# Optimization experiments

Measured on AMD Instinct MI355X. Metric: run time of the kernel, lower is better.

Reference implementation:

```python
import jax, jax.numpy as jnp
import numpy as np

E = 100_000      # number of edges
KMAX = 16        # neighbors (quadruplet basis edges) per edge, exact in this setup
E_NB = E * KMAX  # total neighbor entries
D_EDGE, D_SBF, D_QUAD = 128, 32, 32
INV_SQRT_2 = 0.7071067811865475


def setup_inputs() -> dict:
    key = jax.random.key(0)
    ks = jax.random.split(key, 8)
    m_st = jax.random.normal(ks[0], (E, D_EDGE), dtype=jnp.float32)
    sbf = jax.random.normal(ks[1], (E_NB, D_SBF), dtype=jnp.float32)
    # consistent ragged structure: each edge has exactly KMAX neighbor entries
    edge_nb_idx = jnp.repeat(jnp.arange(E, dtype=jnp.int64), KMAX)
    edge_nb_ragged_idx = jnp.tile(jnp.arange(KMAX, dtype=jnp.int64), E)
    idx_swap = jax.random.permutation(ks[2], E).astype(jnp.int64)
    # parameters (Dense layers are bias-free per the module)
    W_down = jax.random.normal(ks[3], (D_EDGE, D_QUAD), dtype=jnp.float32) / np.sqrt(D_EDGE)
    W_bil = jax.random.normal(ks[4], (D_QUAD, D_SBF, D_QUAD), dtype=jnp.float32) / np.sqrt(D_QUAD * D_SBF)
    W_up_st = jax.random.normal(ks[5], (D_QUAD, D_EDGE), dtype=jnp.float32) / np.sqrt(D_QUAD)
    W_up_ts = jax.random.normal(ks[6], (D_QUAD, D_EDGE), dtype=jnp.float32) / np.sqrt(D_QUAD)
    scale_sbf = jnp.ones((1,), dtype=jnp.float32)  # ScaleFactor (fitted scalar, 1.0 at init)
    return {
        "m_st": m_st, "sbf": sbf, "idx_swap": idx_swap,
        "edge_nb_idx": edge_nb_idx, "edge_nb_ragged_idx": edge_nb_ragged_idx,
        "W_down": W_down, "W_bil": W_bil, "W_up_st": W_up_st,
        "W_up_ts": W_up_ts, "scale_sbf": scale_sbf,
    }


def reference(m_st, sbf, idx_swap, edge_nb_idx, edge_nb_ragged_idx,
              W_down, W_bil, W_up_st, W_up_ts, scale_sbf):
    # mlp_down: Dense(no bias) + SiLU  -> (E, Q)
    m = jax.nn.silu(m_st @ W_down)
    # gather edge embeddings to neighbor entries -> (E_NB, Q)
    m_nb = m[edge_nb_idx]
    # EfficientInteractionBilinear: scatter ragged entries into dense
    # (E, Kmax, *) buffers, then bilinear contraction over neighbors.
    m2 = jnp.zeros((E, KMAX, D_QUAD), m.dtype).at[edge_nb_idx, edge_nb_ragged_idx].set(m_nb)
    s2 = jnp.zeros((E, KMAX, D_SBF), sbf.dtype).at[edge_nb_idx, edge_nb_ragged_idx].set(sbf)
    sum_k = jnp.einsum("eks,ekq->esq", s2, m2)           # (E, S, Q)
    x = jnp.einsum("esq,qso->eo", sum_k, W_bil)          # (E, Q)
    # ScaleFactor: multiply by fitted scalar
    x = x * scale_sbf[0]
    # up-projections + SiLU, swap-add, normalize
    x_st = jax.nn.silu(x @ W_up_st)
    x_ts = jax.nn.silu(x @ W_up_ts)[idx_swap]
    return (x_st + x_ts) * INV_SQRT_2
```

## Files before the change

### kernel.cpp

```cpp
#include <hip/hip_runtime.h>
#include <hip/hip_bf16.h>

#define E_EDGES 100000
#define KMAXN   16
#define D_EDGE  128
#define D_SBF   32
#define D_QUAD  32
#define NTILES  6250

typedef __bf16 bf16x8 __attribute__((ext_vector_type(8)));
typedef float  f32x4  __attribute__((ext_vector_type(4)));

__device__ __forceinline__ float silu_f(float x) {
    return x / (1.0f + __expf(-x));
}

__global__ __launch_bounds__(256) void k012_fused(
        const float* __restrict__ sbf,
        const float* __restrict__ m_st,
        const float* __restrict__ W_down,
        const float* __restrict__ W_bil,
        const float* __restrict__ scale_sbf,
        float* __restrict__ ws_x)
{
    __shared__ __align__(16) __bf16 Blds[32768];
    __shared__ __align__(16) float  Slds[4][512];
    __shared__ __align__(16) float  Mlds[4][512];

    for (int i = threadIdx.x; i < 32768; i += 256) {
        const int q = i >> 10;
        const int rem = i & 1023;
        const int s = rem >> 5;
        const int o = rem & 31;
        Blds[(((s << 2) + (q >> 3)) * 32 + o) * 8 + (q & 7)] = (__bf16)W_bil[i];
    }

    const int lane = threadIdx.x & 63;
    const int n15  = lane & 15;
    const int quad = lane >> 4;
    const int wid  = threadIdx.x >> 6;
    const int wave = blockIdx.x * 4 + wid;
    const int nwav = gridDim.x * 4;
    const int e8   = lane >> 3;
    const int c    = lane & 7;

    bf16x8 bdf[4][2];
    #pragma unroll
    for (int kk = 0; kk < 4; kk++) {
        #pragma unroll
        for (int nt = 0; nt < 2; nt++) {
            bf16x8 b;
            #pragma unroll
            for (int j = 0; j < 8; j++)
                b[j] = (__bf16)W_down[(kk*32 + quad*8 + j) * 32 + nt*16 + n15];
            bdf[kk][nt] = b;
        }
    }

    __syncthreads();

    const float scale = scale_sbf[0];
    float* Sw = Slds[wid];
    float* Mw = Mlds[wid];
    const bf16x8* Bq = (const bf16x8*)Blds;

    for (int tile = wave; tile < NTILES; tile += nwav) {
        const int eb = tile * 16;

        #pragma unroll
        for (int eh = 0; eh < 2; eh++) {
            const float* p = sbf + (size_t)(eb + eh*8 + e8) * (KMAXN * D_SBF) + c * 4;
            float ax = 0.f, ay = 0.f, az = 0.f, aw = 0.f;
            #pragma unroll
            for (int k = 0; k < KMAXN; k++) {
                float4 v = *(const float4*)(p + k * D_SBF);
                ax += v.x; ay += v.y; az += v.z; aw += v.w;
            }
            float4 r = {ax, ay, az, aw};
            *(float4*)(Sw + (eh*8 + e8)*32 + c*4) = r;
        }

        const float* arow = m_st + (size_t)(eb + n15) * 128 + quad * 8;
        f32x4 acc0 = {0.f, 0.f, 0.f, 0.f};
        f32x4 acc1 = {0.f, 0.f, 0.f, 0.f};
        #pragma unroll
        for (int kk = 0; kk < 4; kk++) {
            float4 p0 = *(const float4*)(arow + kk*32);
            float4 p1 = *(const float4*)(arow + kk*32 + 4);
            bf16x8 a;
            a[0]=(__bf16)p0.x; a[1]=(__bf16)p0.y; a[2]=(__bf16)p0.z; a[3]=(__bf16)p0.w;
            a[4]=(__bf16)p1.x; a[5]=(__bf16)p1.y; a[6]=(__bf16)p1.z; a[7]=(__bf16)p1.w;
            acc0 = __builtin_amdgcn_mfma_f32_16x16x32_bf16(a, bdf[kk][0], acc0, 0, 0, 0);
            acc1 = __builtin_amdgcn_mfma_f32_16x16x32_bf16(a, bdf[kk][1], acc1, 0, 0, 0);
        }
        #pragma unroll
        for (int reg = 0; reg < 4; reg++) {
            Mw[(quad*4 + reg)*32 +      n15] = silu_f(acc0[reg]);
            Mw[(quad*4 + reg)*32 + 16 + n15] = silu_f(acc1[reg]);
        }

        asm volatile("s_waitcnt lgkmcnt(0)" ::: "memory");

        const float* mrow = Mw + n15*32 + quad*8;
        float4 m0 = *(const float4*)mrow;
        float4 m1 = *(const float4*)(mrow + 4);
        float mj[8] = {m0.x, m0.y, m0.z, m0.w, m1.x, m1.y, m1.z, m1.w};

        float ss[32];
        const float* srow = Sw + n15*32;
        #pragma unroll
        for (int cc = 0; cc < 8; cc++) {
            float4 v = *(const float4*)(srow + cc*4);
            ss[cc*4+0] = v.x; ss[cc*4+1] = v.y; ss[cc*4+2] = v.z; ss[cc*4+3] = v.w;
        }

        f32x4 xc0 = {0.f, 0.f, 0.f, 0.f};
        f32x4 xc1 = {0.f, 0.f, 0.f, 0.f};
        #pragma unroll
        for (int kk = 0; kk < 32; kk++) {
            const float sv = ss[kk];
            bf16x8 a;
            #pragma unroll
            for (int j = 0; j < 8; j++) a[j] = (__bf16)(sv * mj[j]);
            bf16x8 b0 = Bq[(kk*4 + quad)*32 +      n15];
            bf16x8 b1 = Bq[(kk*4 + quad)*32 + 16 + n15];
            xc0 = __builtin_amdgcn_mfma_f32_16x16x32_bf16(a, b0, xc0, 0, 0, 0);
            xc1 = __builtin_amdgcn_mfma_f32_16x16x32_bf16(a, b1, xc1, 0, 0, 0);
        }

        #pragma unroll
        for (int reg = 0; reg < 4; reg++) {
            const int eo = eb + quad*4 + reg;
            ws_x[(size_t)eo*32 +      n15] = xc0[reg] * scale;
            ws_x[(size_t)eo*32 + 16 + n15] = xc1[reg] * scale;
        }
    }
}

__global__ __launch_bounds__(256) void k3_up(
        const float* __restrict__ ws_x,
        const int*   __restrict__ idx_swap,
        const float* __restrict__ W_up_st,
        const float* __restrict__ W_up_ts,
        float* __restrict__ out)
{
    const int lane = threadIdx.x & 63;
    const int n15  = lane & 15;
    const int quad = lane >> 4;
    const int wave = blockIdx.x * 4 + (threadIdx.x >> 6);
    const int nwav = gridDim.x * 4;

    bf16x8 bst[8], bts[8];
    #pragma unroll
    for (int nt = 0; nt < 8; nt++) {
        bf16x8 a, b;
        #pragma unroll
        for (int j = 0; j < 8; j++) {
            a[j] = (__bf16)W_up_st[(quad*8 + j) * 128 + nt*16 + n15];
            b[j] = (__bf16)W_up_ts[(quad*8 + j) * 128 + nt*16 + n15];
        }
        bst[nt] = a; bts[nt] = b;
    }

    const float cinv = 0.70710678118654752440f;

    for (int tile = wave; tile < NTILES; tile += nwav) {
        const int eb = tile * 16;
        const int e  = eb + n15;
        const int esw = idx_swap[e];

        const float* xr = ws_x + (size_t)e   * 32 + quad * 8;
        const float* xs = ws_x + (size_t)esw * 32 + quad * 8;
        float4 r0 = *(const float4*)xr, r1 = *(const float4*)(xr + 4);
        float4 s0 = *(const float4*)xs, s1 = *(const float4*)(xs + 4);

        bf16x8 ast, ats;
        ast[0]=(__bf16)r0.x; ast[1]=(__bf16)r0.y; ast[2]=(__bf16)r0.z; ast[3]=(__bf16)r0.w;
        ast[4]=(__bf16)r1.x; ast[5]=(__bf16)r1.y; ast[6]=(__bf16)r1.z; ast[7]=(__bf16)r1.w;
        ats[0]=(__bf16)s0.x; ats[1]=(__bf16)s0.y; ats[2]=(__bf16)s0.z; ats[3]=(__bf16)s0.w;
        ats[4]=(__bf16)s1.x; ats[5]=(__bf16)s1.y; ats[6]=(__bf16)s1.z; ats[7]=(__bf16)s1.w;

        f32x4 accst[8], accts[8];
        #pragma unroll
        for (int nt = 0; nt < 8; nt++) {
            f32x4 z = {0.f, 0.f, 0.f, 0.f};
            accst[nt] = __builtin_amdgcn_mfma_f32_16x16x32_bf16(ast, bst[nt], z, 0, 0, 0);
            accts[nt] = __builtin_amdgcn_mfma_f32_16x16x32_bf16(ats, bts[nt], z, 0, 0, 0);
        }

        #pragma unroll
        for (int nt = 0; nt < 8; nt++) {
            #pragma unroll
            for (int reg = 0; reg < 4; reg++) {
                const int eo = eb + quad*4 + reg;
                out[(size_t)eo * 128 + nt*16 + n15] =
                    (silu_f(accst[nt][reg]) + silu_f(accts[nt][reg])) * cinv;
            }
        }
    }
}

extern "C" void kernel_launch(void* const* d_in, const int* in_sizes, int n_in,
                              void* d_out, int out_size, void* d_ws, size_t ws_size,
                              hipStream_t stream)
{
    const float* m_st      = (const float*)d_in[0];
    const float* sbf       = (const float*)d_in[1];
    const int*   idx_swap  = (const int*)  d_in[2];
    const float* W_down    = (const float*)d_in[5];
    const float* W_bil     = (const float*)d_in[6];
    const float* W_up_st   = (const float*)d_in[7];
    const float* W_up_ts   = (const float*)d_in[8];
    const float* scale_sbf = (const float*)d_in[9];
    float* out = (float*)d_out;

    float* ws_x = (float*)d_ws;

    hipLaunchKernelGGL(k012_fused, dim3(512),  dim3(256), 0, stream,
                       sbf, m_st, W_down, W_bil, scale_sbf, ws_x);
    hipLaunchKernelGGL(k3_up,      dim3(1024), dim3(256), 0, stream,
                       ws_x, idx_swap, W_up_st, W_up_ts, out);
}
```

Baseline: 391.9 us.

## Precast weights to bf16 in a prep kernel and launch one tile per wave

A small prep kernel converts W_bil and W_down to bf16 in MFMA-ready layout in workspace. The main kernel no longer stages the 64KB W_bil in LDS per block. It reads B fragments straight from global/L2 and processes one 16-edge tile per wave with a full grid instead of a persistent loop. The LDS staging rows are padded to stride 36 to avoid bank conflicts. This removes the per-block weight conversion and the large LDS footprint, which should allow higher occupancy and overlap of the sbf streaming, at the cost of repeated global reads of the weights and an extra launch.

```diff
diff --git a/kernel.cpp b/kernel.cpp
--- a/kernel.cpp
+++ b/kernel.cpp
@@ -7,6 +7,7 @@
 #define D_SBF   32
 #define D_QUAD  32
 #define NTILES  6250
+#define SP      36
 
 typedef __bf16 bf16x8 __attribute__((ext_vector_type(8)));
 typedef float  f32x4  __attribute__((ext_vector_type(4)));
@@ -15,125 +16,125 @@
     return x / (1.0f + __expf(-x));
 }
 
-__global__ __launch_bounds__(256) void k012_fused(
+__global__ __launch_bounds__(256) void kprep(
+        const float* __restrict__ W_down,
+        const float* __restrict__ W_bil,
+        __bf16* __restrict__ Wd16,
+        __bf16* __restrict__ Wb16)
+{
+    const int t = blockIdx.x * 256 + threadIdx.x;
+    if (t < 4096) {
+        const int o   = t & 31;
+        const int tmp = t >> 5;
+        const int qh  = tmp & 3;
+        const int s   = tmp >> 2;
+        bf16x8 u;
+        #pragma unroll
+        for (int ql = 0; ql < 8; ql++)
+            u[ql] = (__bf16)W_bil[(qh*8 + ql)*1024 + s*32 + o];
+        *(bf16x8*)(Wb16 + (size_t)t * 8) = u;
+    } else if (t < 4096 + 512) {
+        const int t2   = t - 4096;
+        const int n15  = t2 & 15;
+        const int quad = (t2 >> 4) & 3;
+        const int nt   = (t2 >> 6) & 1;
+        const int kk   = t2 >> 7;
+        bf16x8 u;
+        #pragma unroll
+        for (int j = 0; j < 8; j++)
+            u[j] = (__bf16)W_down[(kk*32 + quad*8 + j)*32 + nt*16 + n15];
+        *(bf16x8*)(Wd16 + (size_t)t2 * 8) = u;
+    }
+}
+
+__global__ __launch_bounds__(256, 4) void k012_fused(
         const float* __restrict__ sbf,
         const float* __restrict__ m_st,
-        const float* __restrict__ W_down,
-        const float* __restrict__ W_bil,
+        const __bf16* __restrict__ Wd16,
+        const __bf16* __restrict__ Wb16,
         const float* __restrict__ scale_sbf,
         float* __restrict__ ws_x)
 {
-    __shared__ __align__(16) __bf16 Blds[32768];
-    __shared__ __align__(16) float  Slds[4][512];
-    __shared__ __align__(16) float  Mlds[4][512];
-
-    for (int i = threadIdx.x; i < 32768; i += 256) {
-        const int q = i >> 10;
-        const int rem = i & 1023;
-        const int s = rem >> 5;
-        const int o = rem & 31;
-        Blds[(((s << 2) + (q >> 3)) * 32 + o) * 8 + (q & 7)] = (__bf16)W_bil[i];
-    }
+    __shared__ __align__(16) float Slds[4][16 * SP];
+    __shared__ __align__(16) float Mlds[4][16 * SP];
 
     const int lane = threadIdx.x & 63;
     const int n15  = lane & 15;
     const int quad = lane >> 4;
     const int wid  = threadIdx.x >> 6;
-    const int wave = blockIdx.x * 4 + wid;
-    const int nwav = gridDim.x * 4;
-    const int e8   = lane >> 3;
-    const int c    = lane & 7;
-
-    bf16x8 bdf[4][2];
-    #pragma unroll
-    for (int kk = 0; kk < 4; kk++) {
-        #pragma unroll
-        for (int nt = 0; nt < 2; nt++) {
-            bf16x8 b;
-            #pragma unroll
-            for (int j = 0; j < 8; j++)
-                b[j] = (__bf16)W_down[(kk*32 + quad*8 + j) * 32 + nt*16 + n15];
-            bdf[kk][nt] = b;
-        }
-    }
-
-    __syncthreads();
-
-    const float scale = scale_sbf[0];
+    const int tile = blockIdx.x * 4 + wid;
+    if (tile >= NTILES) return;
+    const int eb = tile * 16;
+    const int e8 = lane >> 3;
+    const int c  = lane & 7;
+
     float* Sw = Slds[wid];
     float* Mw = Mlds[wid];
-    const bf16x8* Bq = (const bf16x8*)Blds;
-
-    for (int tile = wave; tile < NTILES; tile += nwav) {
-        const int eb = tile * 16;
-
-        #pragma unroll
-        for (int eh = 0; eh < 2; eh++) {
-            const float* p = sbf + (size_t)(eb + eh*8 + e8) * (KMAXN * D_SBF) + c * 4;
-            float ax = 0.f, ay = 0.f, az = 0.f, aw = 0.f;
-            #pragma unroll
-            for (int k = 0; k < KMAXN; k++) {
-                float4 v = *(const float4*)(p + k * D_SBF);
-                ax += v.x; ay += v.y; az += v.z; aw += v.w;
-            }
-            float4 r = {ax, ay, az, aw};
-            *(float4*)(Sw + (eh*8 + e8)*32 + c*4) = r;
-        }
-
-        const float* arow = m_st + (size_t)(eb + n15) * 128 + quad * 8;
-        f32x4 acc0 = {0.f, 0.f, 0.f, 0.f};
-        f32x4 acc1 = {0.f, 0.f, 0.f, 0.f};
-        #pragma unroll
-        for (int kk = 0; kk < 4; kk++) {
-            float4 p0 = *(const float4*)(arow + kk*32);
-            float4 p1 = *(const float4*)(arow + kk*32 + 4);
-            bf16x8 a;
-            a[0]=(__bf16)p0.x; a[1]=(__bf16)p0.y; a[2]=(__bf16)p0.z; a[3]=(__bf16)p0.w;
-            a[4]=(__bf16)p1.x; a[5]=(__bf16)p1.y; a[6]=(__bf16)p1.z; a[7]=(__bf16)p1.w;
-            acc0 = __builtin_amdgcn_mfma_f32_16x16x32_bf16(a, bdf[kk][0], acc0, 0, 0, 0);
-            acc1 = __builtin_amdgcn_mfma_f32_16x16x32_bf16(a, bdf[kk][1], acc1, 0, 0, 0);
-        }
-        #pragma unroll
-        for (int reg = 0; reg < 4; reg++) {
-            Mw[(quad*4 + reg)*32 +      n15] = silu_f(acc0[reg]);
-            Mw[(quad*4 + reg)*32 + 16 + n15] = silu_f(acc1[reg]);
-        }
-
-        asm volatile("s_waitcnt lgkmcnt(0)" ::: "memory");
-
-        const float* mrow = Mw + n15*32 + quad*8;
-        float4 m0 = *(const float4*)mrow;
-        float4 m1 = *(const float4*)(mrow + 4);
-        float mj[8] = {m0.x, m0.y, m0.z, m0.w, m1.x, m1.y, m1.z, m1.w};
-
-        float ss[32];
-        const float* srow = Sw + n15*32;
-        #pragma unroll
-        for (int cc = 0; cc < 8; cc++) {
-            float4 v = *(const float4*)(srow + cc*4);
-            ss[cc*4+0] = v.x; ss[cc*4+1] = v.y; ss[cc*4+2] = v.z; ss[cc*4+3] = v.w;
-        }
-
-        f32x4 xc0 = {0.f, 0.f, 0.f, 0.f};
-        f32x4 xc1 = {0.f, 0.f, 0.f, 0.f};
-        #pragma unroll
-        for (int kk = 0; kk < 32; kk++) {
-            const float sv = ss[kk];
-            bf16x8 a;
-            #pragma unroll
-            for (int j = 0; j < 8; j++) a[j] = (__bf16)(sv * mj[j]);
-            bf16x8 b0 = Bq[(kk*4 + quad)*32 +      n15];
-            bf16x8 b1 = Bq[(kk*4 + quad)*32 + 16 + n15];
-            xc0 = __builtin_amdgcn_mfma_f32_16x16x32_bf16(a, b0, xc0, 0, 0, 0);
-            xc1 = __builtin_amdgcn_mfma_f32_16x16x32_bf16(a, b1, xc1, 0, 0, 0);
-        }
-
-        #pragma unroll
-        for (int reg = 0; reg < 4; reg++) {
-            const int eo = eb + quad*4 + reg;
-            ws_x[(size_t)eo*32 +      n15] = xc0[reg] * scale;
-            ws_x[(size_t)eo*32 + 16 + n15] = xc1[reg] * scale;
-        }
+
+    #pragma unroll
+    for (int eh = 0; eh < 2; eh++) {
+        const float* p = sbf + (size_t)(eb + eh*8 + e8) * (KMAXN * D_SBF) + c * 4;
+        float ax = 0.f, ay = 0.f, az = 0.f, aw = 0.f;
+        #pragma unroll
+        for (int k = 0; k < KMAXN; k++) {
+            float4 v = *(const float4*)(p + k * D_SBF);
+            ax += v.x; ay += v.y; az += v.z; aw += v.w;
+        }
+        float4 r = {ax, ay, az, aw};
+        *(float4*)(Sw + (eh*8 + e8) * SP + c * 4) = r;
+    }
+
+    const bf16x8* Wdq = (const bf16x8*)Wd16;
+    const float* arow = m_st + (size_t)(eb + n15) * 128 + quad * 8;
+    f32x4 acc0 = {0.f, 0.f, 0.f, 0.f};
+    f32x4 acc1 = {0.f, 0.f, 0.f, 0.f};
+    #pragma unroll
+    for (int kk = 0; kk < 4; kk++) {
+        float4 p0 = *(const float4*)(arow + kk*32);
+        float4 p1 = *(const float4*)(arow + kk*32 + 4);
+        bf16x8 a;
+        a[0]=(__bf16)p0.x; a[1]=(__bf16)p0.y; a[2]=(__bf16)p0.z; a[3]=(__bf16)p0.w;
+        a[4]=(__bf16)p1.x; a[5]=(__bf16)p1.y; a[6]=(__bf16)p1.z; a[7]=(__bf16)p1.w;
+        bf16x8 b0 = Wdq[(kk*2 + 0)*64 + quad*16 + n15];
+        bf16x8 b1 = Wdq[(kk*2 + 1)*64 + quad*16 + n15];
+        acc0 = __builtin_amdgcn_mfma_f32_16x16x32_bf16(a, b0, acc0, 0, 0, 0);
+        acc1 = __builtin_amdgcn_mfma_f32_16x16x32_bf16(a, b1, acc1, 0, 0, 0);
+    }
+    #pragma unroll
+    for (int reg = 0; reg < 4; reg++) {
+        Mw[(quad*4 + reg)*SP +      n15] = silu_f(acc0[reg]);
+        Mw[(quad*4 + reg)*SP + 16 + n15] = silu_f(acc1[reg]);
+    }
+
+    asm volatile("s_waitcnt lgkmcnt(0)" ::: "memory");
+
+    const float* mrow = Mw + n15*SP + quad*8;
+    float4 m0 = *(const float4*)mrow;
+    float4 m1 = *(const float4*)(mrow + 4);
+    float mj[8] = {m0.x, m0.y, m0.z, m0.w, m1.x, m1.y, m1.z, m1.w};
+    const float* srow = Sw + n15*SP;
+    const bf16x8* Bq = (const bf16x8*)Wb16;
+
+    f32x4 xc0 = {0.f, 0.f, 0.f, 0.f};
+    f32x4 xc1 = {0.f, 0.f, 0.f, 0.f};
+    #pragma unroll
+    for (int kk = 0; kk < 32; kk++) {
+        const float sv = srow[kk];
+        bf16x8 a;
+        #pragma unroll
+        for (int j = 0; j < 8; j++) a[j] = (__bf16)(sv * mj[j]);
+        bf16x8 b0 = Bq[(kk*4 + quad)*32 +      n15];
+        bf16x8 b1 = Bq[(kk*4 + quad)*32 + 16 + n15];
+        xc0 = __builtin_amdgcn_mfma_f32_16x16x32_bf16(a, b0, xc0, 0, 0, 0);
+        xc1 = __builtin_amdgcn_mfma_f32_16x16x32_bf16(a, b1, xc1, 0, 0, 0);
+    }
+
+    const float scale = scale_sbf[0];
+    #pragma unroll
+    for (int reg = 0; reg < 4; reg++) {
+        const int eo = eb + quad*4 + reg;
+        ws_x[(size_t)eo*32 +      n15] = xc0[reg] * scale;
+        ws_x[(size_t)eo*32 + 16 + n15] = xc1[reg] * scale;
     }
 }
 
@@ -214,10 +215,15 @@
     const float* scale_sbf = (const float*)d_in[9];
     float* out = (float*)d_out;
 
-    float* ws_x = (float*)d_ws;
-
-    hipLaunchKernelGGL(k012_fused, dim3(512),  dim3(256), 0, stream,
-                       sbf, m_st, W_down, W_bil, scale_sbf, ws_x);
+    const size_t nEQ = (size_t)E_EDGES * D_QUAD;
+    float*  ws_x = (float*)d_ws;
+    __bf16* Wd16 = (__bf16*)(ws_x + nEQ);
+    __bf16* Wb16 = Wd16 + 512 * 8;
+
+    hipLaunchKernelGGL(kprep,      dim3(18),   dim3(256), 0, stream,
+                       W_down, W_bil, Wd16, Wb16);
+    hipLaunchKernelGGL(k012_fused, dim3(1563), dim3(256), 0, stream,
+                       sbf, m_st, Wd16, Wb16, scale_sbf, ws_x);
     hipLaunchKernelGGL(k3_up,      dim3(1024), dim3(256), 0, stream,
                        ws_x, idx_swap, W_up_st, W_up_ts, out);
 }
```

New measurement: 383.5 us. 1.02x faster.
